# Optimization experiments

Hardware: AMD Instinct MI355X
Metric: run time of the kernel (lower is better)

Reference implementation:

```python
import jax, jax.numpy as jnp
import numpy as np

EMBED = 512
HEADS = 8
EPS = 1e-5


def setup_inputs() -> dict:
    key = jax.random.key(0)
    ks = jax.random.split(key, 8)
    B, Sq, Skv, D = 4, 2048, 2048, EMBED
    return {
        "layer_input": jax.random.normal(ks[0], (B, Sq, D), jnp.float32),
        "cross_attn_input": jax.random.normal(ks[1], (B, Skv, D), jnp.float32),
        "Wq": jax.random.normal(ks[2], (D, D), jnp.float32) * (D ** -0.5),
        "bq": jnp.zeros((D,), jnp.float32),
        "Wkv": jax.random.normal(ks[3], (D, 2 * D), jnp.float32) * (D ** -0.5),
        "bkv": jnp.zeros((2 * D,), jnp.float32),
        "Wo": jax.random.normal(ks[4], (D, D), jnp.float32) * (D ** -0.5),
        "bo": jnp.zeros((D,), jnp.float32),
        "gamma": jnp.ones((D,), jnp.float32),
        "beta": jnp.zeros((D,), jnp.float32),
    }


def _split_heads(x):
    # ... s (h d) -> ... h s d
    *lead, s, hd = x.shape
    d = hd // HEADS
    return jnp.moveaxis(x.reshape(*lead, s, HEADS, d), -2, -3)


def _merge_heads(x):
    # ... h s d -> ... s (h d)
    x = jnp.moveaxis(x, -3, -2)
    *lead, s, h, d = x.shape
    return x.reshape(*lead, s, h * d)


def reference(layer_input, cross_attn_input, Wq, bq, Wkv, bkv, Wo, bo, gamma, beta):
    scale = (EMBED // HEADS) ** -0.5
    res = layer_input
    q = layer_input @ Wq + bq
    kv = cross_attn_input @ Wkv + bkv
    k, v = jnp.split(kv, 2, axis=-1)
    q, k, v = map(_split_heads, (q, k, v))  # [B, H, S, d]
    scores = jnp.einsum('bhqc,bhkc->bhqk', q, k) * scale
    weights = jax.nn.softmax(scores, axis=-1)  # dropout p=0 -> identity
    out = jnp.einsum('bhqk,bhkc->bhqc', weights, v)
    out = _merge_heads(out)
    out = out @ Wo + bo
    x = out + res
    mu = jnp.mean(x, axis=-1, keepdims=True)
    var = jnp.mean(jnp.square(x - mu), axis=-1, keepdims=True)
    return (x - mu) * jax.lax.rsqrt(var + EPS) * gamma + beta
```

## Files before the change

kernel.cpp:

```cpp
#include <hip/hip_runtime.h>
#include <hip/hip_bf16.h>
#include <stdint.h>

#define SEQ    2048
#define DM     512
#define NHEAD  8
#define HD     64
#define BATCH  4
#define MTOT   (BATCH*SEQ)

typedef __attribute__((ext_vector_type(4))) float  f32x4;
typedef __attribute__((ext_vector_type(8))) short  bf16x8;
typedef __attribute__((ext_vector_type(8))) unsigned short u16x8;
typedef __attribute__((ext_vector_type(4))) unsigned short u16x4;
typedef __attribute__((ext_vector_type(4))) float  fl4;
typedef __attribute__((ext_vector_type(2))) unsigned u32x2;
typedef __attribute__((ext_vector_type(4))) unsigned u32x4;

__device__ __forceinline__ unsigned short f2bf(float f) {
  union { float f; unsigned u; } c; c.f = f;
  return (unsigned short)((c.u + 0x7fffu + ((c.u >> 16) & 1u)) >> 16);
}

__device__ __forceinline__ void load_lds16(const void* g, void* l) {
  __builtin_amdgcn_global_load_lds((__attribute__((address_space(1))) void*)g,
                                   (__attribute__((address_space(3))) void*)l,
                                   16, 0, 0);
}

__device__ __forceinline__ u32x2 ds_tr16(const void* p) {
  u32x2 r;
  asm volatile("ds_read_b64_tr_b16 %0, %1"
               : "=v"(r)
               : "v"((__attribute__((address_space(3))) const void*)p));
  return r;
}

__device__ __forceinline__ unsigned pack_bf2(float lo, float hi) {
  __hip_bfloat162 h2 = __float22bfloat162_rn(float2{lo, hi});
  unsigned u; __builtin_memcpy(&u, &h2, 4);
  return u;
}

__global__ void k_pre(const float* __restrict__ X, unsigned short* __restrict__ Xb,
                      const float* __restrict__ C, unsigned short* __restrict__ Cb,
                      const float* __restrict__ Wq, unsigned short* __restrict__ Wqt,
                      const float* __restrict__ Wkv, unsigned short* __restrict__ Wkvt,
                      const float* __restrict__ Wo, unsigned short* __restrict__ Wot) {
  __shared__ __align__(16) unsigned short t[64][66];
  int bid = blockIdx.x, tid = threadIdx.x;
  if (bid < 8192) {
    const float* src = (bid < 4096) ? X : C;
    unsigned short* dst = (bid < 4096) ? Xb : Cb;
    int i = (bid & 4095) * 256 + tid;
    fl4 v = *(const fl4*)(src + (size_t)i * 4);
    u32x2 o;
    o[0] = pack_bf2(v[0], v[1]);
    o[1] = pack_bf2(v[2], v[3]);
    *(u32x2*)((void*)(dst + (size_t)i * 4)) = o;
    return;
  }
  int tjob = bid - 8192;
  const float* W; unsigned short* Wt; int Nd, bx, by;
  if (tjob < 64)       { W = Wq;  Wt = Wqt;  Nd = 512;  bx = tjob & 7;  by = tjob >> 3; }
  else if (tjob < 192) { int u = tjob - 64;  W = Wkv; Wt = Wkvt; Nd = 1024; bx = u & 15; by = u >> 4; }
  else                 { int u = tjob - 192; W = Wo;  Wt = Wot;  Nd = 512;  bx = u & 7;  by = u >> 3; }
  int k0 = by * 64, n0 = bx * 64;
  int r = tid >> 2, cs = (tid & 3) * 16;
  const float* src = W + (size_t)(k0 + r) * Nd + n0 + cs;
#pragma unroll
  for (int i = 0; i < 4; ++i) {
    fl4 v = *(const fl4*)(src + i * 4);
    *(unsigned*)&t[r][cs + i*4]     = pack_bf2(v[0], v[1]);
    *(unsigned*)&t[r][cs + i*4 + 2] = pack_bf2(v[2], v[3]);
  }
  __syncthreads();
  unsigned short* drow = Wt + (size_t)(n0 + r) * 512 + k0 + cs;
#pragma unroll
  for (int half = 0; half < 2; ++half) {
    u16x8 o;
#pragma unroll
    for (int i = 0; i < 8; ++i) o[i] = t[cs + half*8 + i][r];
    *(u16x8*)(drow + half * 8) = o;
  }
}

template<int RESID>
__device__ __forceinline__ void gemm128x64(
    const unsigned short* __restrict__ A,
    const unsigned short* __restrict__ Bt,
    const float* __restrict__ bias,
    const float* __restrict__ res,
    void* __restrict__ Cout,
    int N, int K, int m0, int n0, float osc,
    unsigned short* Als, unsigned short* Bls) {
  int tid  = threadIdx.x;
  int lane = tid & 63, wave = tid >> 6;
  int q = lane & 15, lk = lane >> 4;
  f32x4 acc[2][4];
#pragma unroll
  for (int mt = 0; mt < 2; ++mt)
#pragma unroll
    for (int nt = 0; nt < 4; ++nt) acc[mt][nt] = f32x4{0.f,0.f,0.f,0.f};

  int nkb = K >> 6;
  for (int kb = 0; kb < nkb; ++kb) {
    __syncthreads();
#pragma unroll
    for (int it = 0; it < 4; ++it) {
      int idx = tid + it * 256;
      int row = idx >> 3, ch = idx & 7, sc = ch ^ (row & 7);
      load_lds16(A + (size_t)(m0 + row) * K + kb * 64 + sc * 8,
                 (char*)Als + idx * 16);
    }
#pragma unroll
    for (int it = 0; it < 2; ++it) {
      int idx = tid + it * 256;
      int row = idx >> 3, ch = idx & 7, sc = ch ^ (row & 7);
      load_lds16(Bt + (size_t)(n0 + row) * K + kb * 64 + sc * 8,
                 (char*)Bls + idx * 16);
    }
    __syncthreads();
#pragma unroll
    for (int ks = 0; ks < 2; ++ks) {
      bf16x8 a[2], b[4];
#pragma unroll
      for (int mt = 0; mt < 2; ++mt) {
        int row = wave * 32 + mt * 16 + q;
        a[mt] = *(const bf16x8*)((char*)Als + row * 128 + (((ks*4 + lk) ^ (row & 7)) * 16));
      }
#pragma unroll
      for (int nt = 0; nt < 4; ++nt) {
        int row = nt * 16 + q;
        b[nt] = *(const bf16x8*)((char*)Bls + row * 128 + (((ks*4 + lk) ^ (row & 7)) * 16));
      }
#pragma unroll
      for (int mt = 0; mt < 2; ++mt)
#pragma unroll
        for (int nt = 0; nt < 4; ++nt)
          acc[mt][nt] = __builtin_amdgcn_mfma_f32_16x16x32_bf16(a[mt], b[nt], acc[mt][nt], 0, 0, 0);
    }
  }
#pragma unroll
  for (int nt = 0; nt < 4; ++nt) {
    int col = n0 + nt * 16 + q;
    float bv = bias[col];
#pragma unroll
    for (int mt = 0; mt < 2; ++mt) {
      int rowb = m0 + wave * 32 + mt * 16 + lk * 4;
#pragma unroll
      for (int rr = 0; rr < 4; ++rr) {
        float v = acc[mt][nt][rr] + bv;
        size_t off = (size_t)(rowb + rr) * N + col;
        if (RESID) ((float*)Cout)[off] = v + res[off];
        else       ((unsigned short*)Cout)[off] = f2bf(v * osc);
      }
    }
  }
}

__global__ __launch_bounds__(256, 5)
void k_projmm(const unsigned short* __restrict__ Xb, const unsigned short* __restrict__ Cb,
              const unsigned short* __restrict__ Wqt, const unsigned short* __restrict__ Wkvt,
              const float* __restrict__ bq, const float* __restrict__ bkv,
              unsigned short* __restrict__ Qb, unsigned short* __restrict__ KVb) {
  __shared__ __align__(16) unsigned short Als[128 * 64];
  __shared__ __align__(16) unsigned short Bls[64 * 64];
  int bid = blockIdx.x;
  int l = (bid & 7) * 192 + (bid >> 3);
  const float c1 = 0.125f * 1.44269504088896340736f;
  if (l < 512) {
    int m = l >> 3, n = l & 7;
    gemm128x64<0>(Xb, Wqt, bq, nullptr, Qb, 512, 512, m * 128, n * 64, c1, Als, Bls);
  } else {
    int l2 = l - 512;
    int m = l2 >> 4, n = l2 & 15;
    gemm128x64<0>(Cb, Wkvt, bkv, nullptr, KVb, 1024, 512, m * 128, n * 64, 1.0f, Als, Bls);
  }
}

__global__ __launch_bounds__(256, 4)
void k_omm(const unsigned short* __restrict__ Abuf, const unsigned short* __restrict__ Wot,
           const float* __restrict__ bo, const float* __restrict__ resid,
           float* __restrict__ tmp) {
  __shared__ __align__(16) unsigned short Als[128 * 64];
  __shared__ __align__(16) unsigned short Bls[64 * 64];
  int bid = blockIdx.x;
  int l = (bid & 7) * 64 + (bid >> 3);
  int m = l >> 3, n = l & 7;
  gemm128x64<1>(Abuf, Wot, bo, resid, tmp, 512, 512, m * 128, n * 64, 1.0f, Als, Bls);
}

__global__ __launch_bounds__(256, 4)
void k_attn(const unsigned short* __restrict__ Qb,
            const unsigned short* __restrict__ KVb,
            unsigned short* __restrict__ Ab) {
  __shared__ __align__(16) unsigned short Klds[2][64 * 64];
  __shared__ __align__(16) unsigned short Vlds[3][4096];
  int tid  = threadIdx.x;
  int lane = tid & 63, wave = tid >> 6;
  int q    = lane & 15, lk = lane >> 4;
  int lkb0 = lk & 1, lkb1 = lk >> 1;
  int bid = blockIdx.x;
  int swz = (bid & 7) * 128 + (bid >> 3);
  int qt = swz & 31, bh = swz >> 5;
  int b  = bh >> 3, h = bh & 7;
  int q0 = qt * 64 + wave * 16;
  const size_t kvbase = (size_t)b * SEQ * 1024;

  bf16x8 qf0, qf1;
  {
    size_t qrow = (size_t)b * SEQ + q0 + q;
    qf0 = *(const bf16x8*)(Qb + qrow * DM + h * HD + lk * 8);
    qf1 = *(const bf16x8*)(Qb + qrow * DM + h * HD + 32 + lk * 8);
  }
  f32x4 acc[4];
#pragma unroll
  for (int i = 0; i < 4; ++i) acc[i] = f32x4{0.f,0.f,0.f,0.f};
  float l = 0.f;
  u32x4 pbA[2];

  const unsigned short *gK0, *gK1, *gV0, *gV1;
  {
    int r0 = tid >> 3, s0_ = (tid & 7) ^ (r0 & 7);
    gK0 = KVb + kvbase + (size_t)r0 * 1024 + h * HD + s0_ * 8;
    int i1 = tid + 256, r1 = i1 >> 3, s1_ = (i1 & 7) ^ (r1 & 7);
    gK1 = KVb + kvbase + (size_t)r1 * 1024 + h * HD + s1_ * 8;
    int dt0 = tid >> 7, w0 = tid & 127, p0 = w0 >> 1, c80 = (w0 & 1) * 8;
    int t0 = (p0 & 32) + (((p0 >> 2) & 3) << 3) + (((p0 >> 4) & 1) << 2) + (p0 & 3);
    gV0 = KVb + kvbase + (size_t)t0 * 1024 + 512 + h * HD + dt0 * 16 + c80;
    int i1v = tid + 256, dt1 = i1v >> 7, w1 = i1v & 127, p1 = w1 >> 1, c81 = (w1 & 1) * 8;
    int t1 = (p1 & 32) + (((p1 >> 2) & 3) << 3) + (((p1 >> 4) & 1) << 2) + (p1 & 3);
    gV1 = KVb + kvbase + (size_t)t1 * 1024 + 512 + h * HD + dt1 * 16 + c81;
  }
  char* kdA = (char*)Klds[0] + tid * 16;
  char* kdB = (char*)Klds[1] + tid * 16;
  char* vdA = (char*)Vlds[0] + tid * 16;
  char* vdB = (char*)Vlds[1] + tid * 16;
  char* vdC = (char*)Vlds[2] + tid * 16;
  const char* krA = (const char*)Klds[0];
  const char* krB = (const char*)Klds[1];
  const char* vsA = (const char*)Vlds[0] + lane * 8;
  const char* vsB = (const char*)Vlds[1] + lane * 8;
  const char* vsC = (const char*)Vlds[2] + lane * 8;

#define STAGE(kd_, vd_) do {                        \
    load_lds16(gK0, (kd_));                         \
    load_lds16(gK1, (kd_) + 4096);                  \
    load_lds16(gV0, (vd_));                         \
    load_lds16(gV1, (vd_) + 4096);                  \
    gK0 += 65536; gK1 += 65536;                     \
    gV0 += 65536; gV1 += 65536;                     \
  } while (0)

  STAGE(kdA, vdA);
  __syncthreads();

  const int NT = SEQ / 64;
  int kc = 0;
  int vn = 1;
  int vp = 2;
  for (int kb = 0; kb < NT; ++kb) {
    if (kb < NT - 1) {
      char* kd = kc ? kdA : kdB;
      char* vd = (vn == 0) ? vdA : ((vn == 1) ? vdB : vdC);
      STAGE(kd, vd);
    }

    u32x2 tr[4][2][2];
    if (kb > 0) {
      const char* vsrc = (vp == 0) ? vsA : ((vp == 1) ? vsB : vsC);
#pragma unroll
      for (int dt = 0; dt < 4; ++dt)
#pragma unroll
        for (int ks2 = 0; ks2 < 2; ++ks2)
#pragma unroll
          for (int u = 0; u < 2; ++u)
            tr[dt][ks2][u] = ds_tr16(vsrc + dt * 2048 + ks2 * 1024 + u * 512);
      asm volatile("s_waitcnt lgkmcnt(0)" ::: "memory");
      __builtin_amdgcn_sched_barrier(0);
      __builtin_amdgcn_s_setprio(1);
#pragma unroll
      for (int ks2 = 0; ks2 < 2; ++ks2) {
        union { u32x4 u; bf16x8 v; } pb;
        pb.u = pbA[ks2];
#pragma unroll
        for (int dt = 0; dt < 4; ++dt) {
          union { u32x4 u; bf16x8 v; } cv;
          cv.u[0] = tr[dt][ks2][0][0]; cv.u[1] = tr[dt][ks2][0][1];
          cv.u[2] = tr[dt][ks2][1][0]; cv.u[3] = tr[dt][ks2][1][1];
          acc[dt] = __builtin_amdgcn_mfma_f32_16x16x32_bf16(cv.v, pb.v, acc[dt], 0, 0, 0);
        }
      }
      __builtin_amdgcn_s_setprio(0);
    }

    const char* kr = kc ? krB : krA;
    f32x4 st[4];
#pragma unroll
    for (int kt = 0; kt < 4; ++kt) st[kt] = f32x4{0.f,0.f,0.f,0.f};
    __builtin_amdgcn_s_setprio(1);
#pragma unroll
    for (int kt = 0; kt < 4; ++kt) {
      int row = kt * 16 + q;
      bf16x8 kf0 = *(const bf16x8*)(kr + row * 128 + ((lk ^ (row & 7)) * 16));
      bf16x8 kf1 = *(const bf16x8*)(kr + row * 128 + (((4 + lk) ^ (row & 7)) * 16));
      st[kt] = __builtin_amdgcn_mfma_f32_16x16x32_bf16(kf0, qf0, st[kt], 0, 0, 0);
      st[kt] = __builtin_amdgcn_mfma_f32_16x16x32_bf16(kf1, qf1, st[kt], 0, 0, 0);
    }
    __builtin_amdgcn_s_setprio(0);

    float p[4][4];
#pragma unroll
    for (int kt = 0; kt < 4; ++kt)
#pragma unroll
      for (int r = 0; r < 4; ++r) {
        float pe = __builtin_amdgcn_exp2f(st[kt][r]);
        p[kt][r] = pe;
        l += pe;
      }
    unsigned pk[4][2];
#pragma unroll
    for (int kt = 0; kt < 4; ++kt)
#pragma unroll
      for (int rr = 0; rr < 2; ++rr)
        pk[kt][rr] = pack_bf2(p[kt][2*rr], p[kt][2*rr + 1]);
#pragma unroll
    for (int ks2 = 0; ks2 < 2; ++ks2)
#pragma unroll
      for (int rr = 0; rr < 2; ++rr) {
        unsigned a_ = pk[2*ks2][rr], b_ = pk[2*ks2 + 1][rr];
        unsigned E = lkb1 ? b_ : a_;
        unsigned O = lkb1 ? a_ : b_;
        unsigned A = __shfl_xor((int)E, 16);
        unsigned B = __shfl_xor((int)O, 32);
        unsigned C = __shfl_xor((int)O, 48);
        unsigned dlo = lkb1 ? (lkb0 ? A : B) : (lkb0 ? C : E);
        unsigned dhi = lkb1 ? (lkb0 ? E : C) : (lkb0 ? B : A);
        pbA[ks2][rr]     = dlo;
        pbA[ks2][2 + rr] = dhi;
      }

    __syncthreads();
    kc ^= 1;
    vn = (vn == 2) ? 0 : vn + 1;
    vp = (vp == 2) ? 0 : vp + 1;
  }

  {
    const char* vsrc = (vp == 0) ? vsA : ((vp == 1) ? vsB : vsC);
    u32x2 tr[4][2][2];
#pragma unroll
    for (int dt = 0; dt < 4; ++dt)
#pragma unroll
      for (int ks2 = 0; ks2 < 2; ++ks2)
#pragma unroll
        for (int u = 0; u < 2; ++u)
          tr[dt][ks2][u] = ds_tr16(vsrc + dt * 2048 + ks2 * 1024 + u * 512);
    asm volatile("s_waitcnt lgkmcnt(0)" ::: "memory");
    __builtin_amdgcn_sched_barrier(0);
#pragma unroll
    for (int ks2 = 0; ks2 < 2; ++ks2) {
      union { u32x4 u; bf16x8 v; } pb;
      pb.u = pbA[ks2];
#pragma unroll
      for (int dt = 0; dt < 4; ++dt) {
        union { u32x4 u; bf16x8 v; } cv;
        cv.u[0] = tr[dt][ks2][0][0]; cv.u[1] = tr[dt][ks2][0][1];
        cv.u[2] = tr[dt][ks2][1][0]; cv.u[3] = tr[dt][ks2][1][1];
        acc[dt] = __builtin_amdgcn_mfma_f32_16x16x32_bf16(cv.v, pb.v, acc[dt], 0, 0, 0);
      }
    }
  }

  l += __shfl_xor(l, 16);
  l += __shfl_xor(l, 32);

  float inv = 1.0f / l;
  size_t orow = ((size_t)b * SEQ + q0 + q) * DM + h * HD + lk * 4;
#pragma unroll
  for (int dt = 0; dt < 4; ++dt) {
    u16x4 o;
#pragma unroll
    for (int r = 0; r < 4; ++r) o[r] = f2bf(acc[dt][r] * inv);
    *(u16x4*)(Ab + orow + dt * 16) = o;
  }
#undef STAGE
}

__global__ void k_ln(const float* __restrict__ x, const float* __restrict__ gamma,
                     const float* __restrict__ beta, float* __restrict__ out) {
  int tid = threadIdx.x, lane = tid & 63, wave = tid >> 6;
  size_t row = (size_t)blockIdx.x * 4 + wave;
  const float* xr = x + row * DM + lane * 8;
  fl4 v0 = *(const fl4*)xr;
  fl4 v1 = *(const fl4*)(xr + 4);
  float s  = (v0[0]+v0[1]) + (v0[2]+v0[3]) + (v1[0]+v1[1]) + (v1[2]+v1[3]);
  float ss = (v0[0]*v0[0]+v0[1]*v0[1]) + (v0[2]*v0[2]+v0[3]*v0[3])
           + (v1[0]*v1[0]+v1[1]*v1[1]) + (v1[2]*v1[2]+v1[3]*v1[3]);
#pragma unroll
  for (int off = 1; off < 64; off <<= 1) {
    s  += __shfl_xor(s, off);
    ss += __shfl_xor(ss, off);
  }
  float mu  = s * (1.0f / DM);
  float var = ss * (1.0f / DM) - mu * mu;
  float w = rsqrtf(var + 1e-5f);
  fl4 g0 = *(const fl4*)(gamma + lane*8), g1 = *(const fl4*)(gamma + lane*8 + 4);
  fl4 b0 = *(const fl4*)(beta + lane*8),  b1 = *(const fl4*)(beta + lane*8 + 4);
  fl4 o0, o1;
#pragma unroll
  for (int i = 0; i < 4; ++i) {
    o0[i] = (v0[i] - mu) * w * g0[i] + b0[i];
    o1[i] = (v1[i] - mu) * w * g1[i] + b1[i];
  }
  float* orow = out + row * DM + lane * 8;
  *(fl4*)orow = o0;
  *(fl4*)(orow + 4) = o1;
}

extern "C" void kernel_launch(void* const* d_in, const int* in_sizes, int n_in,
                              void* d_out, int out_size, void* d_ws, size_t ws_size,
                              hipStream_t stream) {
  const float* layer_input = (const float*)d_in[0];
  const float* cross       = (const float*)d_in[1];
  const float* Wq   = (const float*)d_in[2];
  const float* bq   = (const float*)d_in[3];
  const float* Wkv  = (const float*)d_in[4];
  const float* bkv  = (const float*)d_in[5];
  const float* Wo   = (const float*)d_in[6];
  const float* bo   = (const float*)d_in[7];
  const float* gamma = (const float*)d_in[8];
  const float* beta  = (const float*)d_in[9];
  float* out = (float*)d_out;

  char* ws = (char*)d_ws;
  unsigned short* Xb   = (unsigned short*)(ws + (size_t)0);
  unsigned short* Cb   = (unsigned short*)(ws + ((size_t)8  << 20));
  unsigned short* Qb   = (unsigned short*)(ws + ((size_t)16 << 20));
  unsigned short* KVb  = (unsigned short*)(ws + ((size_t)24 << 20));
  unsigned short* Abuf = (unsigned short*)(ws + ((size_t)40 << 20));
  float*          tmp  = (float*)         (ws + ((size_t)48 << 20));
  unsigned short* Wqt  = (unsigned short*)(ws + ((size_t)64 << 20));
  unsigned short* Wkvt = (unsigned short*)(ws + ((size_t)65 << 20));
  unsigned short* Wot  = (unsigned short*)(ws + ((size_t)67 << 20));

  k_pre<<<8448, 256, 0, stream>>>(layer_input, Xb, cross, Cb,
                                  Wq, Wqt, Wkv, Wkvt, Wo, Wot);
  k_projmm<<<1536, 256, 0, stream>>>(Xb, Cb, Wqt, Wkvt, bq, bkv, Qb, KVb);
  k_attn<<<1024, 256, 0, stream>>>(Qb, KVb, Abuf);
  k_omm<<<512, 256, 0, stream>>>(Abuf, Wot, bo, layer_input, tmp);
  k_ln<<<MTOT/4, 256, 0, stream>>>(tmp, gamma, beta, out);
}
```

Baseline: 116.7 us.

## Double-buffer LDS tiles in projection and output GEMMs to overlap loads

The shared GEMM helper now uses two LDS buffers for the A and B tiles. It prefetches the next K-block with async global-to-LDS loads while MFMAs run on the current one, and needs only one barrier per iteration instead of two. Global pointers are precomputed and advanced incrementally. LDS per block doubles, so the launch-bound occupancy hints are lowered to 3 for both GEMM kernels, which trades occupancy for in-block latency hiding.

```diff
diff --git a/kernel.cpp b/kernel.cpp
--- a/kernel.cpp
+++ b/kernel.cpp
@@ -103,36 +103,54 @@
 #pragma unroll
     for (int nt = 0; nt < 4; ++nt) acc[mt][nt] = f32x4{0.f,0.f,0.f,0.f};
 
+  const unsigned short* gA[4];
+#pragma unroll
+  for (int it = 0; it < 4; ++it) {
+    int idx = tid + it * 256;
+    int row = idx >> 3, ch = idx & 7, sc = ch ^ (row & 7);
+    gA[it] = A + (size_t)(m0 + row) * K + sc * 8;
+  }
+  const unsigned short* gB[2];
+#pragma unroll
+  for (int it = 0; it < 2; ++it) {
+    int idx = tid + it * 256;
+    int row = idx >> 3, ch = idx & 7, sc = ch ^ (row & 7);
+    gB[it] = Bt + (size_t)(n0 + row) * K + sc * 8;
+  }
+  char* aD = (char*)Als + tid * 16;
+  char* bD = (char*)Bls + tid * 16;
+
+#pragma unroll
+  for (int it = 0; it < 4; ++it) { load_lds16(gA[it], aD + it * 4096); gA[it] += 64; }
+#pragma unroll
+  for (int it = 0; it < 2; ++it) { load_lds16(gB[it], bD + it * 4096); gB[it] += 64; }
+  __syncthreads();
+
   int nkb = K >> 6;
+  int buf = 0;
   for (int kb = 0; kb < nkb; ++kb) {
-    __syncthreads();
-#pragma unroll
-    for (int it = 0; it < 4; ++it) {
-      int idx = tid + it * 256;
-      int row = idx >> 3, ch = idx & 7, sc = ch ^ (row & 7);
-      load_lds16(A + (size_t)(m0 + row) * K + kb * 64 + sc * 8,
-                 (char*)Als + idx * 16);
-    }
-#pragma unroll
-    for (int it = 0; it < 2; ++it) {
-      int idx = tid + it * 256;
-      int row = idx >> 3, ch = idx & 7, sc = ch ^ (row & 7);
-      load_lds16(Bt + (size_t)(n0 + row) * K + kb * 64 + sc * 8,
-                 (char*)Bls + idx * 16);
-    }
-    __syncthreads();
+    if (kb + 1 < nkb) {
+      char* aN = aD + (buf ^ 1) * 16384;
+      char* bN = bD + (buf ^ 1) * 8192;
+#pragma unroll
+      for (int it = 0; it < 4; ++it) { load_lds16(gA[it], aN + it * 4096); gA[it] += 64; }
+#pragma unroll
+      for (int it = 0; it < 2; ++it) { load_lds16(gB[it], bN + it * 4096); gB[it] += 64; }
+    }
+    const char* aR = (const char*)Als + buf * 16384;
+    const char* bR = (const char*)Bls + buf * 8192;
 #pragma unroll
     for (int ks = 0; ks < 2; ++ks) {
       bf16x8 a[2], b[4];
 #pragma unroll
       for (int mt = 0; mt < 2; ++mt) {
         int row = wave * 32 + mt * 16 + q;
-        a[mt] = *(const bf16x8*)((char*)Als + row * 128 + (((ks*4 + lk) ^ (row & 7)) * 16));
+        a[mt] = *(const bf16x8*)(aR + row * 128 + (((ks*4 + lk) ^ (row & 7)) * 16));
       }
 #pragma unroll
       for (int nt = 0; nt < 4; ++nt) {
         int row = nt * 16 + q;
-        b[nt] = *(const bf16x8*)((char*)Bls + row * 128 + (((ks*4 + lk) ^ (row & 7)) * 16));
+        b[nt] = *(const bf16x8*)(bR + row * 128 + (((ks*4 + lk) ^ (row & 7)) * 16));
       }
 #pragma unroll
       for (int mt = 0; mt < 2; ++mt)
@@ -140,6 +158,8 @@
         for (int nt = 0; nt < 4; ++nt)
           acc[mt][nt] = __builtin_amdgcn_mfma_f32_16x16x32_bf16(a[mt], b[nt], acc[mt][nt], 0, 0, 0);
     }
+    __syncthreads();
+    buf ^= 1;
   }
 #pragma unroll
   for (int nt = 0; nt < 4; ++nt) {
@@ -159,13 +179,13 @@
   }
 }
 
-__global__ __launch_bounds__(256, 5)
+__global__ __launch_bounds__(256, 3)
 void k_projmm(const unsigned short* __restrict__ Xb, const unsigned short* __restrict__ Cb,
               const unsigned short* __restrict__ Wqt, const unsigned short* __restrict__ Wkvt,
               const float* __restrict__ bq, const float* __restrict__ bkv,
               unsigned short* __restrict__ Qb, unsigned short* __restrict__ KVb) {
-  __shared__ __align__(16) unsigned short Als[128 * 64];
-  __shared__ __align__(16) unsigned short Bls[64 * 64];
+  __shared__ __align__(16) unsigned short Als[2 * 128 * 64];
+  __shared__ __align__(16) unsigned short Bls[2 * 64 * 64];
   int bid = blockIdx.x;
   int l = (bid & 7) * 192 + (bid >> 3);
   const float c1 = 0.125f * 1.44269504088896340736f;
@@ -179,12 +199,12 @@
   }
 }
 
-__global__ __launch_bounds__(256, 4)
+__global__ __launch_bounds__(256, 3)
 void k_omm(const unsigned short* __restrict__ Abuf, const unsigned short* __restrict__ Wot,
            const float* __restrict__ bo, const float* __restrict__ resid,
            float* __restrict__ tmp) {
-  __shared__ __align__(16) unsigned short Als[128 * 64];
-  __shared__ __align__(16) unsigned short Bls[64 * 64];
+  __shared__ __align__(16) unsigned short Als[2 * 128 * 64];
+  __shared__ __align__(16) unsigned short Bls[2 * 64 * 64];
   int bid = blockIdx.x;
   int l = (bid & 7) * 64 + (bid >> 3);
   int m = l >> 3, n = l & 7;
```

Measured after the change: 116.1 us. Within noise of the previous version (-0.5%).
